# Optimization experiments

Hardware: AMD Instinct MI355X
Metric: run time of the kernel (lower is better)

The kernel has to match this reference:

```python
import jax, jax.numpy as jnp
import numpy as np

SIGMA_BOOST = 2.0   # sparse-hyper util.SIGMA_BOOST
EPSILON = 1e-6      # sparse-hyper util.EPSILON (10e-7)
B, N = 512, 16384   # batch, size


def setup_inputs() -> dict:
    key = jax.random.key(0)
    k1, k2, k3, k4, k5 = jax.random.split(key, 5)
    return {
        "x": jax.random.normal(k1, (B, N), jnp.float32),
        "noise": jax.random.normal(k2, (B, N, 2), jnp.float32),
        "pmeans": jax.random.normal(k3, (N, 2), jnp.float32),
        "psigmas": jax.random.normal(k4, (N,), jnp.float32),
        "pvalues": jax.random.normal(k5, (N,), jnp.float32),
    }


def reference(x, noise, pmeans, psigmas, pvalues):
    b, n = x.shape
    s = jnp.float32(n)  # square size (n, n); both dims equal
    # hyper(): transform_means = sigmoid * (size-1); transform_sigmas = (softplus(.+boost)+eps) * size
    means = jax.nn.sigmoid(pmeans)[None] * (s - 1.0)                    # (1, n, 2) -> bcast (b, n, 2)
    sigmas = (jax.nn.softplus(psigmas + SIGMA_BOOST) + EPSILON)[None, :, None] * s  # (1, n, 1)
    # Normal(means, sigmas).sample() -- non-differentiable sample
    samples = jax.lax.stop_gradient(means + sigmas * noise)             # (b, n, 2)
    # round, clamp to [0, n-1]
    indices = jnp.clip(jnp.round(samples).astype(jnp.int32), 0, n - 1)  # (b, n, 2)
    rows, cols = indices[..., 0], indices[..., 1]                       # (b, n) each
    values = jnp.broadcast_to(pvalues[None, :], (b, n))
    # sparse.contract: y[b, rows[b,t]] += values[b,t] * x[b, cols[b,t]]
    contrib = values * jnp.take_along_axis(x, cols, axis=1)             # (b, n)
    y = jnp.zeros((b, n), x.dtype).at[jnp.arange(b)[:, None], rows].add(contrib)
    return y
```

## Files before the change

### kernel.cpp

```cpp
#include <hip/hip_runtime.h>
#include <math.h>

#define SIGMA_BOOST 2.0f
#define EPSILON 1e-6f

__global__ void params_kernel(const float2* __restrict__ pmeans,
                              const float* __restrict__ psigmas,
                              const float* __restrict__ pvalues,
                              float4* __restrict__ params, int N) {
    int t = blockIdx.x * blockDim.x + threadIdx.x;
    if (t >= N) return;
    float2 pm = pmeans[t];
    float scale = (float)(N - 1);
    float m0 = __fmul_rn(__fdiv_rn(1.0f, __fadd_rn(1.0f, expf(-pm.x))), scale);
    float m1 = __fmul_rn(__fdiv_rn(1.0f, __fadd_rn(1.0f, expf(-pm.y))), scale);
    float z  = __fadd_rn(psigmas[t], SIGMA_BOOST);
    float sp = __fadd_rn(fmaxf(z, 0.0f), log1pf(expf(-fabsf(z))));
    float sg = __fmul_rn(__fadd_rn(sp, EPSILON), (float)N);
    params[t] = make_float4(m0, m1, sg, pvalues[t]);
}

template <bool INLINE_PARAMS>
__launch_bounds__(1024, 1)
__global__ void contract_kernel(const float* __restrict__ x,
                                const float2* __restrict__ noise,
                                const float4* __restrict__ params,
                                const float2* __restrict__ pmeans,
                                const float* __restrict__ psigmas,
                                const float* __restrict__ pvalues,
                                float* __restrict__ y, int N) {
    extern __shared__ float ly[];
    const int b = blockIdx.x;
    const int tid = threadIdx.x;
    const int nthr = blockDim.x;

    float4* ly4 = (float4*)ly;
    const int n4 = N >> 2;
    for (int i = tid; i < n4; i += nthr) ly4[i] = make_float4(0.f, 0.f, 0.f, 0.f);
    __syncthreads();

    const float*  xb = x + (size_t)b * N;
    const float2* nb = noise + (size_t)b * N;
    const float fN1 = (float)(N - 1);

    for (int t = tid; t < N; t += nthr) {
        float m0, m1, sg, pv;
        if (INLINE_PARAMS) {
            float2 pm = pmeans[t];
            float scale = (float)(N - 1);
            m0 = __fmul_rn(__fdiv_rn(1.0f, __fadd_rn(1.0f, expf(-pm.x))), scale);
            m1 = __fmul_rn(__fdiv_rn(1.0f, __fadd_rn(1.0f, expf(-pm.y))), scale);
            float z  = __fadd_rn(psigmas[t], SIGMA_BOOST);
            float sp = __fadd_rn(fmaxf(z, 0.0f), log1pf(expf(-fabsf(z))));
            sg = __fmul_rn(__fadd_rn(sp, EPSILON), (float)N);
            pv = pvalues[t];
        } else {
            float4 p = params[t];
            m0 = p.x; m1 = p.y; sg = p.z; pv = p.w;
        }
        float2 nz = nb[t];
        float s0 = __fadd_rn(m0, __fmul_rn(sg, nz.x));
        float s1 = __fadd_rn(m1, __fmul_rn(sg, nz.y));
        int row = (int)fminf(fmaxf(rintf(s0), 0.0f), fN1);
        int col = (int)fminf(fmaxf(rintf(s1), 0.0f), fN1);
        float contrib = __fmul_rn(pv, xb[col]);
        atomicAdd(&ly[row], contrib);
    }
    __syncthreads();

    float4* yb4 = (float4*)(y + (size_t)b * N);
    for (int i = tid; i < n4; i += nthr) yb4[i] = ly4[i];
}

extern "C" void kernel_launch(void* const* d_in, const int* in_sizes, int n_in,
                              void* d_out, int out_size, void* d_ws, size_t ws_size,
                              hipStream_t stream) {
    const float*  x       = (const float*)d_in[0];
    const float2* noise   = (const float2*)d_in[1];
    const float2* pmeans  = (const float2*)d_in[2];
    const float*  psigmas = (const float*)d_in[3];
    const float*  pvalues = (const float*)d_in[4];
    float* y = (float*)d_out;

    const int N = in_sizes[3];
    const int B = in_sizes[0] / N;

    const size_t params_bytes = (size_t)N * sizeof(float4);
    const bool use_ws = (ws_size >= params_bytes) && (d_ws != nullptr);

    const int block = 1024;
    const size_t lds_bytes = (size_t)N * sizeof(float);

    if (use_ws) {
        float4* params = (float4*)d_ws;
        params_kernel<<<(N + 255) / 256, 256, 0, stream>>>(pmeans, psigmas,
                                                           pvalues, params, N);
        contract_kernel<false><<<B, block, lds_bytes, stream>>>(
            x, noise, params, nullptr, nullptr, nullptr, y, N);
    } else {
        contract_kernel<true><<<B, block, lds_bytes, stream>>>(
            x, noise, nullptr, pmeans, psigmas, pvalues, y, N);
    }
}
```

Measured before the change: 164.0 us.

## Vectorize noise loads, unroll four elements per thread, use nontemporal streaming

The contract kernel now has a fast path in which each thread handles four elements per iteration. It loads noise as 16-byte vectors with nontemporal hints, reads four params entries, and issues four independent gathers and LDS atomics. The output store becomes nontemporal, and the launch-bounds occupancy hint rises from 1 to 8. The aim is wider noise loads, more memory-level parallelism, and less cache pollution from single-use streams; the cost is higher register pressure, and the hint may constrain register allocation.

```diff
diff --git a/kernel.cpp b/kernel.cpp
--- a/kernel.cpp
+++ b/kernel.cpp
@@ -3,6 +3,8 @@
 
 #define SIGMA_BOOST 2.0f
 #define EPSILON 1e-6f
+
+typedef float vfloat4 __attribute__((ext_vector_type(4)));
 
 __global__ void params_kernel(const float2* __restrict__ pmeans,
                               const float* __restrict__ psigmas,
@@ -21,7 +23,7 @@
 }
 
 template <bool INLINE_PARAMS>
-__launch_bounds__(1024, 1)
+__launch_bounds__(1024, 8)
 __global__ void contract_kernel(const float* __restrict__ x,
                                 const float2* __restrict__ noise,
                                 const float4* __restrict__ params,
@@ -39,37 +41,82 @@
     for (int i = tid; i < n4; i += nthr) ly4[i] = make_float4(0.f, 0.f, 0.f, 0.f);
     __syncthreads();
 
-    const float*  xb = x + (size_t)b * N;
-    const float2* nb = noise + (size_t)b * N;
+    const float* xb = x + (size_t)b * N;
     const float fN1 = (float)(N - 1);
 
-    for (int t = tid; t < N; t += nthr) {
-        float m0, m1, sg, pv;
-        if (INLINE_PARAMS) {
-            float2 pm = pmeans[t];
-            float scale = (float)(N - 1);
-            m0 = __fmul_rn(__fdiv_rn(1.0f, __fadd_rn(1.0f, expf(-pm.x))), scale);
-            m1 = __fmul_rn(__fdiv_rn(1.0f, __fadd_rn(1.0f, expf(-pm.y))), scale);
-            float z  = __fadd_rn(psigmas[t], SIGMA_BOOST);
-            float sp = __fadd_rn(fmaxf(z, 0.0f), log1pf(expf(-fabsf(z))));
-            sg = __fmul_rn(__fadd_rn(sp, EPSILON), (float)N);
-            pv = pvalues[t];
-        } else {
-            float4 p = params[t];
-            m0 = p.x; m1 = p.y; sg = p.z; pv = p.w;
+    if (!INLINE_PARAMS && (N % (4 * nthr)) == 0) {
+        const vfloat4* nb4 = (const vfloat4*)(noise + (size_t)b * N);
+        const int npairs = N >> 1;
+        for (int base = 0; base < npairs; base += 2 * nthr) {
+            const int p0 = base + tid;
+            const int p1 = base + nthr + tid;
+            vfloat4 nz0 = __builtin_nontemporal_load(&nb4[p0]);
+            vfloat4 nz1 = __builtin_nontemporal_load(&nb4[p1]);
+            float4 pa = params[2 * p0];
+            float4 pb = params[2 * p0 + 1];
+            float4 pc = params[2 * p1];
+            float4 pd = params[2 * p1 + 1];
+
+            float sA0 = __fadd_rn(pa.x, __fmul_rn(pa.z, nz0.x));
+            float sA1 = __fadd_rn(pa.y, __fmul_rn(pa.z, nz0.y));
+            float sB0 = __fadd_rn(pb.x, __fmul_rn(pb.z, nz0.z));
+            float sB1 = __fadd_rn(pb.y, __fmul_rn(pb.z, nz0.w));
+            float sC0 = __fadd_rn(pc.x, __fmul_rn(pc.z, nz1.x));
+            float sC1 = __fadd_rn(pc.y, __fmul_rn(pc.z, nz1.y));
+            float sD0 = __fadd_rn(pd.x, __fmul_rn(pd.z, nz1.z));
+            float sD1 = __fadd_rn(pd.y, __fmul_rn(pd.z, nz1.w));
+
+            int rA = (int)fminf(fmaxf(rintf(sA0), 0.0f), fN1);
+            int cA = (int)fminf(fmaxf(rintf(sA1), 0.0f), fN1);
+            int rB = (int)fminf(fmaxf(rintf(sB0), 0.0f), fN1);
+            int cB = (int)fminf(fmaxf(rintf(sB1), 0.0f), fN1);
+            int rC = (int)fminf(fmaxf(rintf(sC0), 0.0f), fN1);
+            int cC = (int)fminf(fmaxf(rintf(sC1), 0.0f), fN1);
+            int rD = (int)fminf(fmaxf(rintf(sD0), 0.0f), fN1);
+            int cD = (int)fminf(fmaxf(rintf(sD1), 0.0f), fN1);
+
+            float xA = xb[cA];
+            float xB = xb[cB];
+            float xC = xb[cC];
+            float xD = xb[cD];
+
+            atomicAdd(&ly[rA], __fmul_rn(pa.w, xA));
+            atomicAdd(&ly[rB], __fmul_rn(pb.w, xB));
+            atomicAdd(&ly[rC], __fmul_rn(pc.w, xC));
+            atomicAdd(&ly[rD], __fmul_rn(pd.w, xD));
         }
-        float2 nz = nb[t];
-        float s0 = __fadd_rn(m0, __fmul_rn(sg, nz.x));
-        float s1 = __fadd_rn(m1, __fmul_rn(sg, nz.y));
-        int row = (int)fminf(fmaxf(rintf(s0), 0.0f), fN1);
-        int col = (int)fminf(fmaxf(rintf(s1), 0.0f), fN1);
-        float contrib = __fmul_rn(pv, xb[col]);
-        atomicAdd(&ly[row], contrib);
+    } else {
+        const float2* nb = noise + (size_t)b * N;
+        for (int t = tid; t < N; t += nthr) {
+            float m0, m1, sg, pv;
+            if (INLINE_PARAMS) {
+                float2 pm = pmeans[t];
+                float scale = (float)(N - 1);
+                m0 = __fmul_rn(__fdiv_rn(1.0f, __fadd_rn(1.0f, expf(-pm.x))), scale);
+                m1 = __fmul_rn(__fdiv_rn(1.0f, __fadd_rn(1.0f, expf(-pm.y))), scale);
+                float z  = __fadd_rn(psigmas[t], SIGMA_BOOST);
+                float sp = __fadd_rn(fmaxf(z, 0.0f), log1pf(expf(-fabsf(z))));
+                sg = __fmul_rn(__fadd_rn(sp, EPSILON), (float)N);
+                pv = pvalues[t];
+            } else {
+                float4 p = params[t];
+                m0 = p.x; m1 = p.y; sg = p.z; pv = p.w;
+            }
+            float2 nz = nb[t];
+            float s0 = __fadd_rn(m0, __fmul_rn(sg, nz.x));
+            float s1 = __fadd_rn(m1, __fmul_rn(sg, nz.y));
+            int row = (int)fminf(fmaxf(rintf(s0), 0.0f), fN1);
+            int col = (int)fminf(fmaxf(rintf(s1), 0.0f), fN1);
+            float contrib = __fmul_rn(pv, xb[col]);
+            atomicAdd(&ly[row], contrib);
+        }
     }
     __syncthreads();
 
-    float4* yb4 = (float4*)(y + (size_t)b * N);
-    for (int i = tid; i < n4; i += nthr) yb4[i] = ly4[i];
+    const vfloat4* lv4 = (const vfloat4*)ly;
+    vfloat4* yb4 = (vfloat4*)(y + (size_t)b * N);
+    for (int i = tid; i < n4; i += nthr)
+        __builtin_nontemporal_store(lv4[i], &yb4[i]);
 }
 
 extern "C" void kernel_launch(void* const* d_in, const int* in_sizes, int n_in,
```

Result: no change. 161.8 us (-1.3%).

## Privatize boundary-bin accumulation and vectorize noise loads with nontemporal hints

Applied to the files above, without the earlier changes.

Rows and columns that clamp to 0 or N-1 are handled specially. Their x values are read once and cached in registers, and their contributions are summed per thread, reduced across each wavefront, and added once per wave. This avoids heavy LDS atomic contention on the two clamp bins. Noise is now read as 16-byte nontemporal loads with two samples per thread-iteration, and output is written with nontemporal stores. The launch-bounds occupancy hint is also raised, which may constrain register allocation.

```diff
diff --git a/kernel.cpp b/kernel.cpp
--- a/kernel.cpp
+++ b/kernel.cpp
@@ -3,6 +3,8 @@
 
 #define SIGMA_BOOST 2.0f
 #define EPSILON 1e-6f
+
+typedef float vfloat4 __attribute__((ext_vector_type(4)));
 
 __global__ void params_kernel(const float2* __restrict__ pmeans,
                               const float* __restrict__ psigmas,
@@ -20,8 +22,27 @@
     params[t] = make_float4(m0, m1, sg, pvalues[t]);
 }
 
+__device__ __forceinline__ void process_sample(
+        const float4 p, const float n0, const float n1,
+        const float* __restrict__ xb, float* __restrict__ ly,
+        const float x0, const float xE, const int iN1, const float fN1,
+        float& acc0, float& accE) {
+    float s0 = __fadd_rn(p.x, __fmul_rn(p.z, n0));
+    float s1 = __fadd_rn(p.y, __fmul_rn(p.z, n1));
+    int row = (int)fminf(fmaxf(rintf(s0), 0.0f), fN1);
+    int col = (int)fminf(fmaxf(rintf(s1), 0.0f), fN1);
+    float xv;
+    if (col == 0)        xv = x0;
+    else if (col == iN1) xv = xE;
+    else                 xv = xb[col];
+    float ctr = __fmul_rn(p.w, xv);
+    if (row == 0)        acc0 = __fadd_rn(acc0, ctr);
+    else if (row == iN1) accE = __fadd_rn(accE, ctr);
+    else                 atomicAdd(&ly[row], ctr);
+}
+
 template <bool INLINE_PARAMS>
-__launch_bounds__(1024, 1)
+__launch_bounds__(1024, 8)
 __global__ void contract_kernel(const float* __restrict__ x,
                                 const float2* __restrict__ noise,
                                 const float4* __restrict__ params,
@@ -39,37 +60,66 @@
     for (int i = tid; i < n4; i += nthr) ly4[i] = make_float4(0.f, 0.f, 0.f, 0.f);
     __syncthreads();
 
-    const float*  xb = x + (size_t)b * N;
-    const float2* nb = noise + (size_t)b * N;
+    const float* xb = x + (size_t)b * N;
     const float fN1 = (float)(N - 1);
+    const int iN1 = N - 1;
+    const float x0 = xb[0];
+    const float xE = xb[iN1];
+    float acc0 = 0.0f, accE = 0.0f;
 
-    for (int t = tid; t < N; t += nthr) {
-        float m0, m1, sg, pv;
-        if (INLINE_PARAMS) {
-            float2 pm = pmeans[t];
-            float scale = (float)(N - 1);
-            m0 = __fmul_rn(__fdiv_rn(1.0f, __fadd_rn(1.0f, expf(-pm.x))), scale);
-            m1 = __fmul_rn(__fdiv_rn(1.0f, __fadd_rn(1.0f, expf(-pm.y))), scale);
-            float z  = __fadd_rn(psigmas[t], SIGMA_BOOST);
-            float sp = __fadd_rn(fmaxf(z, 0.0f), log1pf(expf(-fabsf(z))));
-            sg = __fmul_rn(__fadd_rn(sp, EPSILON), (float)N);
-            pv = pvalues[t];
-        } else {
-            float4 p = params[t];
-            m0 = p.x; m1 = p.y; sg = p.z; pv = p.w;
+    if (!INLINE_PARAMS && ((N >> 1) % (2 * nthr)) == 0) {
+        const vfloat4* nb4 = (const vfloat4*)(noise + (size_t)b * N);
+        const int npairs = N >> 1;
+        for (int base = 0; base < npairs; base += 2 * nthr) {
+            const int p0 = base + tid;
+            const int p1 = p0 + nthr;
+            vfloat4 nz0 = __builtin_nontemporal_load(&nb4[p0]);
+            vfloat4 nz1 = __builtin_nontemporal_load(&nb4[p1]);
+            float4 pa = params[2 * p0];
+            float4 pb = params[2 * p0 + 1];
+            float4 pc = params[2 * p1];
+            float4 pd = params[2 * p1 + 1];
+
+            process_sample(pa, nz0.x, nz0.y, xb, ly, x0, xE, iN1, fN1, acc0, accE);
+            process_sample(pb, nz0.z, nz0.w, xb, ly, x0, xE, iN1, fN1, acc0, accE);
+            process_sample(pc, nz1.x, nz1.y, xb, ly, x0, xE, iN1, fN1, acc0, accE);
+            process_sample(pd, nz1.z, nz1.w, xb, ly, x0, xE, iN1, fN1, acc0, accE);
         }
-        float2 nz = nb[t];
-        float s0 = __fadd_rn(m0, __fmul_rn(sg, nz.x));
-        float s1 = __fadd_rn(m1, __fmul_rn(sg, nz.y));
-        int row = (int)fminf(fmaxf(rintf(s0), 0.0f), fN1);
-        int col = (int)fminf(fmaxf(rintf(s1), 0.0f), fN1);
-        float contrib = __fmul_rn(pv, xb[col]);
-        atomicAdd(&ly[row], contrib);
+    } else {
+        const float2* nb = noise + (size_t)b * N;
+        for (int t = tid; t < N; t += nthr) {
+            float4 p;
+            if (INLINE_PARAMS) {
+                float2 pm = pmeans[t];
+                float scale = (float)(N - 1);
+                p.x = __fmul_rn(__fdiv_rn(1.0f, __fadd_rn(1.0f, expf(-pm.x))), scale);
+                p.y = __fmul_rn(__fdiv_rn(1.0f, __fadd_rn(1.0f, expf(-pm.y))), scale);
+                float z  = __fadd_rn(psigmas[t], SIGMA_BOOST);
+                float sp = __fadd_rn(fmaxf(z, 0.0f), log1pf(expf(-fabsf(z))));
+                p.z = __fmul_rn(__fadd_rn(sp, EPSILON), (float)N);
+                p.w = pvalues[t];
+            } else {
+                p = params[t];
+            }
+            float2 nz = nb[t];
+            process_sample(p, nz.x, nz.y, xb, ly, x0, xE, iN1, fN1, acc0, accE);
+        }
+    }
+
+    for (int off = 32; off > 0; off >>= 1) {
+        acc0 = __fadd_rn(acc0, __shfl_down(acc0, off, 64));
+        accE = __fadd_rn(accE, __shfl_down(accE, off, 64));
+    }
+    if ((tid & 63) == 0) {
+        atomicAdd(&ly[0], acc0);
+        atomicAdd(&ly[iN1], accE);
     }
     __syncthreads();
 
-    float4* yb4 = (float4*)(y + (size_t)b * N);
-    for (int i = tid; i < n4; i += nthr) yb4[i] = ly4[i];
+    const vfloat4* lv4 = (const vfloat4*)ly;
+    vfloat4* yb4 = (vfloat4*)(y + (size_t)b * N);
+    for (int i = tid; i < n4; i += nthr)
+        __builtin_nontemporal_store(lv4[i], &yb4[i]);
 }
 
 extern "C" void kernel_launch(void* const* d_in, const int* in_sizes, int n_in,
```

Result: faster. 149.9 us (-8.6%).
